# Kernel tuning notes

Measured on AMD Instinct MI355X. Metric: run time of the kernel, lower is better.

Reference implementation:

```python
import jax, jax.numpy as jnp
import numpy as np

CLS_NUM = 2
SCALE = 8.0
NO_OBJ_SCALE = 1.0
EPS = 1e-7


def setup_inputs() -> dict:
    key = jax.random.key(0)
    k1, k2, k3, k4, k5, k6 = jax.random.split(key, 6)
    B, C, H, W, N = 8, CLS_NUM, 512, 512, 160
    predict = jax.random.normal(k1, (B, C, H, W), dtype=jnp.float32)
    b = jax.random.randint(k2, (N,), 0, B).astype(jnp.float32)
    c = jax.random.randint(k3, (N,), 0, C).astype(jnp.float32)
    cxy = jax.random.uniform(k4, (N, 2), minval=0.0, maxval=H * SCALE)
    wh = jax.random.uniform(k5, (N, 2), minval=64.0, maxval=256.0)
    ang = jax.random.uniform(k6, (N, 1), minval=-np.pi, maxval=np.pi)
    targets = jnp.concatenate([b[:, None], c[:, None], cxy, wh, ang], axis=1).astype(jnp.float32)
    return {"predict": predict, "targets": targets}


def _forward(predict, targets):
    B, C, H, W = predict.shape
    pred = jnp.transpose(predict, (0, 2, 3, 1))          # [B,H,W,C]
    conf_all = jax.nn.sigmoid(pred)
    heatmap = jnp.max(conf_all, axis=-1)                 # [B,H,W]

    bid = targets[:, 0].astype(jnp.int32)                # [N] batch ids
    cid = targets[:, 1].astype(jnp.int32)                # [N] class ids
    cx = targets[:, 2] / SCALE
    cy = targets[:, 3] / SCALE
    w = targets[:, 4] / SCALE
    h = targets[:, 5] / SCALE
    ang = targets[:, 6]
    cos, sin = jnp.cos(ang), jnp.sin(ang)
    # rotate box center into the rotated frame (same math as render_map)
    x = cx * cos + cy * sin
    y = -cx * sin + cy * cos
    x3, x4 = x - h / 2, x + h / 2
    y3, y4 = y - w / 2, y + w / 2
    x1, x2 = x3 - 0.5, x4 + 0.5
    y1, y2 = y3 - 0.5, y4 + 0.5

    gx = jnp.arange(W, dtype=jnp.float32)[None, :] + 0.5  # [1,W] -> broadcasts to [H,W]
    gy = jnp.arange(H, dtype=jnp.float32)[:, None] + 0.5  # [H,1]
    vx = cos[:, None, None] * gx + sin[:, None, None] * gy   # [N,H,W]
    vy = -sin[:, None, None] * gx + cos[:, None, None] * gy  # [N,H,W]

    def box_mask(lo_x, hi_x, lo_y, hi_y):
        return ((lo_x[:, None, None] <= vx) & (vx <= hi_x[:, None, None]) &
                (lo_y[:, None, None] <= vy) & (vy <= hi_y[:, None, None]))

    inner = box_mask(x3, x4, y3, y4)  # obj region, [N,H,W]
    outer = box_mask(x1, x2, y1, y2)  # expanded region (clears noobj)

    loss = jnp.float32(0.0)
    for cls in range(CLS_NUM):
        sel = (cid == cls)[:, None, None]
        obj_cnt = jax.ops.segment_sum((inner & sel).astype(jnp.float32), bid, num_segments=B)
        out_cnt = jax.ops.segment_sum((outer & sel).astype(jnp.float32), bid, num_segments=B)
        obj_mask = obj_cnt > 0            # [B,H,W]
        noobj_mask = out_cnt <= 0         # starts at 1, zeroed inside any expanded box
        conf_c = jnp.clip(conf_all[..., cls], EPS, 1.0 - EPS)
        n_obj = jnp.sum(obj_mask)
        n_noobj = jnp.sum(noobj_mask)
        # BCE with target 1 on obj cells, target 0 on noobj cells (tconf == obj mask)
        loss_obj = -jnp.sum(jnp.where(obj_mask, jnp.log(conf_c), 0.0)) / jnp.maximum(n_obj, 1)
        loss_noobj = -jnp.sum(jnp.where(noobj_mask, jnp.log(1.0 - conf_c), 0.0)) / jnp.maximum(n_noobj, 1)
        loss = loss + jnp.where(n_obj > 0, loss_obj + NO_OBJ_SCALE * loss_noobj, 0.0)
    return loss, heatmap


def reference(predict, targets):
    return _forward(predict, targets)
```

## Files before the change

kernel.cpp:

```cpp
#include <hip/hip_runtime.h>
#include <math.h>

#define CLS 2
#define BATCH 8
#define HH 512
#define WW 512
#define INV_SCALE 0.125f
#define LOGEPS -16.118095651f

#define MAXT 256
#define NBLK 2048


__global__ __launch_bounds__(256) void heatmap_main(
    const float* __restrict__ predict, const float* __restrict__ targets,
    int nT, float* __restrict__ out,
    double* __restrict__ gsumd, int* __restrict__ gcnti)
{
    __shared__ float s_cs[MAXT], s_sn[MAXT], s_x3[MAXT], s_x4[MAXT],
                     s_y3[MAXT], s_y4[MAXT];
    __shared__ int s_cid[MAXT];
    __shared__ int s_nb;
    __shared__ double s_bs[4][4];
    __shared__ int s_bc[4][2];

    const int tid = threadIdx.x;
    const int blockPix = blockIdx.x << 10;
    const int b = blockPix >> 18;

    if (tid == 0) s_nb = 0;
    __syncthreads();
    for (int t0 = tid; t0 < nT; t0 += 256) {
        const float* tp = targets + t0 * 7;
        if ((int)tp[0] == b) {
            const float cs = cosf(tp[6]), sn = sinf(tp[6]);
            const float cx = tp[2] * INV_SCALE, cy = tp[3] * INV_SCALE;
            const float w_ = tp[4] * INV_SCALE, h_ = tp[5] * INV_SCALE;
            const float x =  cx * cs + cy * sn;
            const float y = -cx * sn + cy * cs;
            const int slot = atomicAdd(&s_nb, 1);
            s_cs[slot] = cs; s_sn[slot] = sn;
            s_x3[slot] = x - 0.5f * h_; s_x4[slot] = x + 0.5f * h_;
            s_y3[slot] = y - 0.5f * w_; s_y4[slot] = y + 0.5f * w_;
            s_cid[slot] = (int)tp[1];
        }
    }
    __syncthreads();
    const int nb = s_nb;

    const int wid = tid >> 6;
    const int l   = tid & 63;
    const int spix = blockPix + (wid << 8);
    const int i  = (spix >> 9) & (HH - 1);
    const int j0 = spix & (WW - 1);
    const float gy = (float)i + 0.5f;
    const int j = j0 + 4 * l;
    const float gxb = (float)j + 0.5f;

    int objm[4] = {0, 0, 0, 0}, outm[4] = {0, 0, 0, 0};

    for (int base = 0; base < nb; base += 64) {
        const int t = base + l;
        bool acc = false;
        if (t < nb) {
            const float cs = s_cs[t], sn = s_sn[t];
            const float gxl = (float)j0 + 0.5f, gxh = (float)j0 + 255.5f;
            const float a1 = cs * gxl + sn * gy, a2 = cs * gxh + sn * gy;
            const float b1 = -sn * gxl + cs * gy, b2 = -sn * gxh + cs * gy;
            const float vxlo = fminf(a1, a2), vxhi = fmaxf(a1, a2);
            const float vylo = fminf(b1, b2), vyhi = fmaxf(b1, b2);
            const float M = 0.51f;
            acc = (vxhi >= s_x3[t] - M) & (vxlo <= s_x4[t] + M) &
                  (vyhi >= s_y3[t] - M) & (vylo <= s_y4[t] + M);
        }
        unsigned long long bal = __ballot(acc);
        while (bal) {
            const int n = base + __builtin_ctzll(bal);
            bal &= bal - 1;
            const float ccs = s_cs[n], csn = s_sn[n];
            const float cx3 = s_x3[n], cx4 = s_x4[n];
            const float cy3 = s_y3[n], cy4 = s_y4[n];
            const int cbit = 1 << s_cid[n];
            float vx =  ccs * gxb + csn * gy;
            float vy = -csn * gxb + ccs * gy;
            #pragma unroll
            for (int k = 0; k < 4; ++k) {
                const bool in_  = (cx3 <= vx) & (vx <= cx4) &
                                  (cy3 <= vy) & (vy <= cy4);
                const bool out_ = (cx3 - 0.5f <= vx) & (vx <= cx4 + 0.5f) &
                                  (cy3 - 0.5f <= vy) & (vy <= cy4 + 0.5f);
                if (in_)  objm[k] |= cbit;
                if (out_) outm[k] |= cbit;
                vx += ccs; vy -= csn;
            }
        }
    }

    const int pbase = (b * CLS * HH + i) * WW + j;
    const float4 P0 = *(const float4*)(predict + pbase);
    const float4 P1 = *(const float4*)(predict + pbase + HH * WW);

    float so0 = 0.f, so1 = 0.f, sq0 = 0.f, sq1 = 0.f;
    int c_obj0 = 0, c_obj1 = 0, c_no0 = 0, c_no1 = 0;
    float hm[4];
    #pragma unroll
    for (int k = 0; k < 4; ++k) {
        const float p0 = (&P0.x)[k], p1 = (&P1.x)[k];
        const float t0 = __expf(p0), t1 = __expf(p1);
        const float l0n = -__logf(1.0f + t0);
        const float l1n = -__logf(1.0f + t1);
        const float lc0 = fmaxf(p0 + l0n, LOGEPS);
        const float lc1 = fmaxf(p1 + l1n, LOGEPS);
        const float l0c = fmaxf(l0n, LOGEPS);
        const float l1c = fmaxf(l1n, LOGEPS);
        const float tm = fmaxf(t0, t1);
        hm[k] = tm * __builtin_amdgcn_rcpf(1.0f + tm);
        const int om = objm[k], um = outm[k];
        if (om & 1) { so0 += lc0; ++c_obj0; }
        if (om & 2) { so1 += lc1; ++c_obj1; }
        if (!(um & 1)) { sq0 += l0c; ++c_no0; }
        if (!(um & 2)) { sq1 += l1c; ++c_no1; }
    }

    float* ho = out + 1 + (b * HH + i) * WW + j;
    ho[0] = hm[0]; ho[1] = hm[1]; ho[2] = hm[2]; ho[3] = hm[3];

    const unsigned long long anyobj =
        __ballot((objm[0] | objm[1] | objm[2] | objm[3]) != 0);
    int pc = (c_no0 & 0xffff) | (c_no1 << 16);
    #pragma unroll
    for (int off = 32; off >= 1; off >>= 1) {
        sq0 += __shfl_down(sq0, off);
        sq1 += __shfl_down(sq1, off);
        pc  += __shfl_down(pc, off);
    }
    int po = 0;
    if (anyobj) {
        po = (c_obj0 & 0xffff) | (c_obj1 << 16);
        #pragma unroll
        for (int off = 32; off >= 1; off >>= 1) {
            so0 += __shfl_down(so0, off);
            so1 += __shfl_down(so1, off);
            po  += __shfl_down(po, off);
        }
    }
    if (l == 0) {
        s_bs[wid][0] = (double)so0; s_bs[wid][1] = (double)so1;
        s_bs[wid][2] = (double)sq0; s_bs[wid][3] = (double)sq1;
        s_bc[wid][0] = po;          s_bc[wid][1] = pc;
    }
    __syncthreads();
    if (tid == 0) {
        double o0 = 0, o1 = 0, q0 = 0, q1 = 0;
        int P = 0, Q = 0;
        #pragma unroll
        for (int w = 0; w < 4; ++w) {
            o0 += s_bs[w][0]; o1 += s_bs[w][1];
            q0 += s_bs[w][2]; q1 += s_bs[w][3];
            P  += s_bc[w][0]; Q  += s_bc[w][1];
        }
        const int blk = blockIdx.x;
        gsumd[0 * NBLK + blk] = o0; gsumd[1 * NBLK + blk] = o1;
        gsumd[2 * NBLK + blk] = q0; gsumd[3 * NBLK + blk] = q1;
        gcnti[0 * NBLK + blk] = P;  gcnti[1 * NBLK + blk] = Q;
    }
}

__global__ __launch_bounds__(512) void heatmap_finalize(
    const double* __restrict__ gsumd, const int* __restrict__ gcnti,
    float* __restrict__ out)
{
    const int t = threadIdx.x;
    double f[4] = {0, 0, 0, 0};
    int co0 = 0, co1 = 0, cn0 = 0, cn1 = 0;
    for (int blk = t; blk < NBLK; blk += 512) {
        #pragma unroll
        for (int q = 0; q < 4; ++q) f[q] += gsumd[q * NBLK + blk];
        const int p = gcnti[0 * NBLK + blk];
        const int q2 = gcnti[1 * NBLK + blk];
        co0 += p & 0xffff;  co1 += p >> 16;
        cn0 += q2 & 0xffff; cn1 += q2 >> 16;
    }
    #pragma unroll
    for (int off = 32; off >= 1; off >>= 1) {
        #pragma unroll
        for (int q = 0; q < 4; ++q) f[q] += __shfl_down(f[q], off);
        co0 += __shfl_down(co0, off); co1 += __shfl_down(co1, off);
        cn0 += __shfl_down(cn0, off); cn1 += __shfl_down(cn1, off);
    }

    __shared__ double sf[8][4];
    __shared__ int    sc[8][4];
    const int wv = t >> 6, ln = t & 63;
    if (ln == 0) {
        #pragma unroll
        for (int q = 0; q < 4; ++q) sf[wv][q] = f[q];
        sc[wv][0] = co0; sc[wv][1] = co1; sc[wv][2] = cn0; sc[wv][3] = cn1;
    }
    __syncthreads();
    if (t == 0) {
        double F[4] = {0, 0, 0, 0}; int C[4] = {0, 0, 0, 0};
        for (int w = 0; w < 8; ++w)
            #pragma unroll
            for (int q = 0; q < 4; ++q) { F[q] += sf[w][q]; C[q] += sc[w][q]; }
        float loss = 0.0f;
        if (C[0] > 0)
            loss += -(float)F[0] / (float)C[0]
                    - (float)F[2] / (float)(C[2] > 0 ? C[2] : 1);
        if (C[1] > 0)
            loss += -(float)F[1] / (float)C[1]
                    - (float)F[3] / (float)(C[3] > 0 ? C[3] : 1);
        out[0] = loss;
    }
}

extern "C" void kernel_launch(void* const* d_in, const int* in_sizes, int n_in,
                              void* d_out, int out_size, void* d_ws, size_t ws_size,
                              hipStream_t stream) {
    const float* predict = (const float*)d_in[0];
    const float* targets = (const float*)d_in[1];
    const int nT = in_sizes[1] / 7;
    float* out = (float*)d_out;
    char* ws = (char*)d_ws;
    double* gsumd = (double*)ws;
    int* gcnti = (int*)(ws + 65536);

    heatmap_main<<<NBLK, 256, 0, stream>>>(predict, targets, nT, out,
                                           gsumd, gcnti);
    heatmap_finalize<<<1, 512, 0, stream>>>(gsumd, gcnti, out);
}
```

Measured before the change: 79.15 us.

## Fuse finalize into main kernel via cooperative grid sync; process 8 pixels per lane

Each block now covers 2048 pixels as four full rows, so a lane handles eight pixels and the grid shrinks to 1024 blocks. The box culling test runs per whole row instead of per half row. The noobj sum is now taken unconditionally and then corrected only for pixels inside any box, and log is computed with log2. When the device supports it, a cooperative launch with a grid sync lets block 0 do the final reduction, removing the second kernel launch. This relies on all 1024 blocks being co-resident at occupancy 4, pays for the grid barrier, and halves the block count, which may reduce latency hiding.

```diff
diff --git a/kernel.cpp b/kernel.cpp
--- a/kernel.cpp
+++ b/kernel.cpp
@@ -1,4 +1,5 @@
 #include <hip/hip_runtime.h>
+#include <hip/hip_cooperative_groups.h>
 #include <math.h>
 
 #define CLS 2
@@ -7,12 +8,16 @@
 #define WW 512
 #define INV_SCALE 0.125f
 #define LOGEPS -16.118095651f
-
-#define MAXT 256
-#define NBLK 2048
-
-
-__global__ __launch_bounds__(256) void heatmap_main(
+#define NLN2 -0.69314718056f
+
+#define MAXT 192
+#define NBLK 1024
+
+namespace cg = cooperative_groups;
+
+
+template <bool COOP>
+__global__ __launch_bounds__(256, 4) void heatmap_main(
     const float* __restrict__ predict, const float* __restrict__ targets,
     int nT, float* __restrict__ out,
     double* __restrict__ gsumd, int* __restrict__ gcnti)
@@ -22,10 +27,10 @@
     __shared__ int s_cid[MAXT];
     __shared__ int s_nb;
     __shared__ double s_bs[4][4];
-    __shared__ int s_bc[4][2];
+    __shared__ int s_bc[4][4];
 
     const int tid = threadIdx.x;
-    const int blockPix = blockIdx.x << 10;
+    const int blockPix = blockIdx.x << 11;
     const int b = blockPix >> 18;
 
     if (tid == 0) s_nb = 0;
@@ -48,25 +53,21 @@
     __syncthreads();
     const int nb = s_nb;
 
-    const int wid = tid >> 6;
-    const int l   = tid & 63;
-    const int spix = blockPix + (wid << 8);
-    const int i  = (spix >> 9) & (HH - 1);
-    const int j0 = spix & (WW - 1);
+    const int wid = tid >> 6, l = tid & 63;
+    const int i = ((blockPix >> 9) + wid) & (HH - 1);
     const float gy = (float)i + 0.5f;
-    const int j = j0 + 4 * l;
+    const int j = l << 3;
     const float gxb = (float)j + 0.5f;
 
-    int objm[4] = {0, 0, 0, 0}, outm[4] = {0, 0, 0, 0};
+    int objp = 0, outp = 0;
 
     for (int base = 0; base < nb; base += 64) {
         const int t = base + l;
         bool acc = false;
         if (t < nb) {
             const float cs = s_cs[t], sn = s_sn[t];
-            const float gxl = (float)j0 + 0.5f, gxh = (float)j0 + 255.5f;
-            const float a1 = cs * gxl + sn * gy, a2 = cs * gxh + sn * gy;
-            const float b1 = -sn * gxl + cs * gy, b2 = -sn * gxh + cs * gy;
+            const float a1 = cs * 0.5f + sn * gy,  a2 = cs * 511.5f + sn * gy;
+            const float b1 = -sn * 0.5f + cs * gy, b2 = -sn * 511.5f + cs * gy;
             const float vxlo = fminf(a1, a2), vxhi = fmaxf(a1, a2);
             const float vylo = fminf(b1, b2), vyhi = fmaxf(b1, b2);
             const float M = 0.51f;
@@ -80,54 +81,63 @@
             const float ccs = s_cs[n], csn = s_sn[n];
             const float cx3 = s_x3[n], cx4 = s_x4[n];
             const float cy3 = s_y3[n], cy4 = s_y4[n];
-            const int cbit = 1 << s_cid[n];
+            const float ox3 = cx3 - 0.5f, ox4 = cx4 + 0.5f;
+            const float oy3 = cy3 - 0.5f, oy4 = cy4 + 0.5f;
+            const int cb = 1 << s_cid[n];
             float vx =  ccs * gxb + csn * gy;
             float vy = -csn * gxb + ccs * gy;
             #pragma unroll
-            for (int k = 0; k < 4; ++k) {
+            for (int k = 0; k < 8; ++k) {
                 const bool in_  = (cx3 <= vx) & (vx <= cx4) &
                                   (cy3 <= vy) & (vy <= cy4);
-                const bool out_ = (cx3 - 0.5f <= vx) & (vx <= cx4 + 0.5f) &
-                                  (cy3 - 0.5f <= vy) & (vy <= cy4 + 0.5f);
-                if (in_)  objm[k] |= cbit;
-                if (out_) outm[k] |= cbit;
+                const bool out_ = (ox3 <= vx) & (vx <= ox4) &
+                                  (oy3 <= vy) & (vy <= oy4);
+                if (in_)  objp |= cb << (2 * k);
+                if (out_) outp |= cb << (2 * k);
                 vx += ccs; vy -= csn;
             }
         }
     }
 
     const int pbase = (b * CLS * HH + i) * WW + j;
-    const float4 P0 = *(const float4*)(predict + pbase);
-    const float4 P1 = *(const float4*)(predict + pbase + HH * WW);
-
-    float so0 = 0.f, so1 = 0.f, sq0 = 0.f, sq1 = 0.f;
-    int c_obj0 = 0, c_obj1 = 0, c_no0 = 0, c_no1 = 0;
-    float hm[4];
+    const float4 A0 = *(const float4*)(predict + pbase);
+    const float4 A1 = *(const float4*)(predict + pbase + 4);
+    const float4 B0 = *(const float4*)(predict + pbase + HH * WW);
+    const float4 B1 = *(const float4*)(predict + pbase + HH * WW + 4);
+    float p0[8], p1[8];
+    p0[0]=A0.x; p0[1]=A0.y; p0[2]=A0.z; p0[3]=A0.w;
+    p0[4]=A1.x; p0[5]=A1.y; p0[6]=A1.z; p0[7]=A1.w;
+    p1[0]=B0.x; p1[1]=B0.y; p1[2]=B0.z; p1[3]=B0.w;
+    p1[4]=B1.x; p1[5]=B1.y; p1[6]=B1.z; p1[7]=B1.w;
+
+    float l0n[8], l1n[8];
+    float sq0 = 0.f, sq1 = 0.f;
+    float* ho = out + 1 + (b * HH + i) * WW + j;
     #pragma unroll
-    for (int k = 0; k < 4; ++k) {
-        const float p0 = (&P0.x)[k], p1 = (&P1.x)[k];
-        const float t0 = __expf(p0), t1 = __expf(p1);
-        const float l0n = -__logf(1.0f + t0);
-        const float l1n = -__logf(1.0f + t1);
-        const float lc0 = fmaxf(p0 + l0n, LOGEPS);
-        const float lc1 = fmaxf(p1 + l1n, LOGEPS);
-        const float l0c = fmaxf(l0n, LOGEPS);
-        const float l1c = fmaxf(l1n, LOGEPS);
+    for (int k = 0; k < 8; ++k) {
+        const float t0 = __expf(p0[k]);
+        const float t1 = __expf(p1[k]);
+        l0n[k] = __log2f(1.0f + t0) * NLN2;
+        l1n[k] = __log2f(1.0f + t1) * NLN2;
+        sq0 += fmaxf(l0n[k], LOGEPS);
+        sq1 += fmaxf(l1n[k], LOGEPS);
         const float tm = fmaxf(t0, t1);
-        hm[k] = tm * __builtin_amdgcn_rcpf(1.0f + tm);
-        const int om = objm[k], um = outm[k];
-        if (om & 1) { so0 += lc0; ++c_obj0; }
-        if (om & 2) { so1 += lc1; ++c_obj1; }
-        if (!(um & 1)) { sq0 += l0c; ++c_no0; }
-        if (!(um & 2)) { sq1 += l1c; ++c_no1; }
-    }
-
-    float* ho = out + 1 + (b * HH + i) * WW + j;
-    ho[0] = hm[0]; ho[1] = hm[1]; ho[2] = hm[2]; ho[3] = hm[3];
-
-    const unsigned long long anyobj =
-        __ballot((objm[0] | objm[1] | objm[2] | objm[3]) != 0);
-    int pc = (c_no0 & 0xffff) | (c_no1 << 16);
+        ho[k] = tm * __builtin_amdgcn_rcpf(1.0f + tm);
+    }
+    int cn0 = 8, cn1 = 8, co0 = 0, co1 = 0;
+    float so0 = 0.f, so1 = 0.f;
+    if (outp) {
+        #pragma unroll
+        for (int k = 0; k < 8; ++k) {
+            if (outp & (1 << (2 * k))) { sq0 -= fmaxf(l0n[k], LOGEPS); --cn0; }
+            if (outp & (2 << (2 * k))) { sq1 -= fmaxf(l1n[k], LOGEPS); --cn1; }
+            if (objp & (1 << (2 * k))) { so0 += fmaxf(p0[k] + l0n[k], LOGEPS); ++co0; }
+            if (objp & (2 << (2 * k))) { so1 += fmaxf(p1[k] + l1n[k], LOGEPS); ++co1; }
+        }
+    }
+
+    const unsigned long long anyobj = __ballot(objp != 0);
+    int pc = (cn0 & 0xffff) | (cn1 << 16);
     #pragma unroll
     for (int off = 32; off >= 1; off >>= 1) {
         sq0 += __shfl_down(sq0, off);
@@ -136,7 +146,7 @@
     }
     int po = 0;
     if (anyobj) {
-        po = (c_obj0 & 0xffff) | (c_obj1 << 16);
+        po = (co0 & 0xffff) | (co1 << 16);
         #pragma unroll
         for (int off = 32; off >= 1; off >>= 1) {
             so0 += __shfl_down(so0, off);
@@ -163,46 +173,97 @@
         gsumd[0 * NBLK + blk] = o0; gsumd[1 * NBLK + blk] = o1;
         gsumd[2 * NBLK + blk] = q0; gsumd[3 * NBLK + blk] = q1;
         gcnti[0 * NBLK + blk] = P;  gcnti[1 * NBLK + blk] = Q;
+        __threadfence();
+    }
+
+    if (COOP) {
+        cg::this_grid().sync();
+        if (blockIdx.x == 0) {
+            __threadfence();
+            double f0 = 0, f1 = 0, f2 = 0, f3 = 0;
+            int c0 = 0, c1 = 0, c2 = 0, c3 = 0;
+            for (int blk = tid; blk < NBLK; blk += 256) {
+                f0 += gsumd[0 * NBLK + blk]; f1 += gsumd[1 * NBLK + blk];
+                f2 += gsumd[2 * NBLK + blk]; f3 += gsumd[3 * NBLK + blk];
+                const int P = gcnti[0 * NBLK + blk];
+                const int Q = gcnti[1 * NBLK + blk];
+                c0 += P & 0xffff; c1 += (int)((unsigned)P >> 16);
+                c2 += Q & 0xffff; c3 += (int)((unsigned)Q >> 16);
+            }
+            #pragma unroll
+            for (int off = 32; off >= 1; off >>= 1) {
+                f0 += __shfl_down(f0, off); f1 += __shfl_down(f1, off);
+                f2 += __shfl_down(f2, off); f3 += __shfl_down(f3, off);
+                c0 += __shfl_down(c0, off); c1 += __shfl_down(c1, off);
+                c2 += __shfl_down(c2, off); c3 += __shfl_down(c3, off);
+            }
+            const int wv = tid >> 6, ln = tid & 63;
+            if (ln == 0) {
+                s_bs[wv][0] = f0; s_bs[wv][1] = f1;
+                s_bs[wv][2] = f2; s_bs[wv][3] = f3;
+                s_bc[wv][0] = c0; s_bc[wv][1] = c1;
+                s_bc[wv][2] = c2; s_bc[wv][3] = c3;
+            }
+            __syncthreads();
+            if (tid == 0) {
+                double F[4] = {0, 0, 0, 0}; int C[4] = {0, 0, 0, 0};
+                for (int w = 0; w < 4; ++w) {
+                    F[0] += s_bs[w][0]; F[1] += s_bs[w][1];
+                    F[2] += s_bs[w][2]; F[3] += s_bs[w][3];
+                    C[0] += s_bc[w][0]; C[1] += s_bc[w][1];
+                    C[2] += s_bc[w][2]; C[3] += s_bc[w][3];
+                }
+                float loss = 0.0f;
+                if (C[0] > 0)
+                    loss += -(float)F[0] / (float)C[0]
+                            - (float)F[2] / (float)(C[2] > 0 ? C[2] : 1);
+                if (C[1] > 0)
+                    loss += -(float)F[1] / (float)C[1]
+                            - (float)F[3] / (float)(C[3] > 0 ? C[3] : 1);
+                out[0] = loss;
+            }
+        }
     }
 }
 
-__global__ __launch_bounds__(512) void heatmap_finalize(
+__global__ __launch_bounds__(256) void heatmap_finalize(
     const double* __restrict__ gsumd, const int* __restrict__ gcnti,
     float* __restrict__ out)
 {
+    __shared__ double sf[4][4];
+    __shared__ int    sc[4][4];
     const int t = threadIdx.x;
-    double f[4] = {0, 0, 0, 0};
-    int co0 = 0, co1 = 0, cn0 = 0, cn1 = 0;
-    for (int blk = t; blk < NBLK; blk += 512) {
-        #pragma unroll
-        for (int q = 0; q < 4; ++q) f[q] += gsumd[q * NBLK + blk];
-        const int p = gcnti[0 * NBLK + blk];
-        const int q2 = gcnti[1 * NBLK + blk];
-        co0 += p & 0xffff;  co1 += p >> 16;
-        cn0 += q2 & 0xffff; cn1 += q2 >> 16;
+    double f0 = 0, f1 = 0, f2 = 0, f3 = 0;
+    int c0 = 0, c1 = 0, c2 = 0, c3 = 0;
+    for (int blk = t; blk < NBLK; blk += 256) {
+        f0 += gsumd[0 * NBLK + blk]; f1 += gsumd[1 * NBLK + blk];
+        f2 += gsumd[2 * NBLK + blk]; f3 += gsumd[3 * NBLK + blk];
+        const int P = gcnti[0 * NBLK + blk];
+        const int Q = gcnti[1 * NBLK + blk];
+        c0 += P & 0xffff; c1 += (int)((unsigned)P >> 16);
+        c2 += Q & 0xffff; c3 += (int)((unsigned)Q >> 16);
     }
     #pragma unroll
     for (int off = 32; off >= 1; off >>= 1) {
-        #pragma unroll
-        for (int q = 0; q < 4; ++q) f[q] += __shfl_down(f[q], off);
-        co0 += __shfl_down(co0, off); co1 += __shfl_down(co1, off);
-        cn0 += __shfl_down(cn0, off); cn1 += __shfl_down(cn1, off);
-    }
-
-    __shared__ double sf[8][4];
-    __shared__ int    sc[8][4];
+        f0 += __shfl_down(f0, off); f1 += __shfl_down(f1, off);
+        f2 += __shfl_down(f2, off); f3 += __shfl_down(f3, off);
+        c0 += __shfl_down(c0, off); c1 += __shfl_down(c1, off);
+        c2 += __shfl_down(c2, off); c3 += __shfl_down(c3, off);
+    }
     const int wv = t >> 6, ln = t & 63;
     if (ln == 0) {
-        #pragma unroll
-        for (int q = 0; q < 4; ++q) sf[wv][q] = f[q];
-        sc[wv][0] = co0; sc[wv][1] = co1; sc[wv][2] = cn0; sc[wv][3] = cn1;
+        sf[wv][0] = f0; sf[wv][1] = f1; sf[wv][2] = f2; sf[wv][3] = f3;
+        sc[wv][0] = c0; sc[wv][1] = c1; sc[wv][2] = c2; sc[wv][3] = c3;
     }
     __syncthreads();
     if (t == 0) {
         double F[4] = {0, 0, 0, 0}; int C[4] = {0, 0, 0, 0};
-        for (int w = 0; w < 8; ++w)
-            #pragma unroll
-            for (int q = 0; q < 4; ++q) { F[q] += sf[w][q]; C[q] += sc[w][q]; }
+        for (int w = 0; w < 4; ++w) {
+            F[0] += sf[w][0]; F[1] += sf[w][1];
+            F[2] += sf[w][2]; F[3] += sf[w][3];
+            C[0] += sc[w][0]; C[1] += sc[w][1];
+            C[2] += sc[w][2]; C[3] += sc[w][3];
+        }
         float loss = 0.0f;
         if (C[0] > 0)
             loss += -(float)F[0] / (float)C[0]
@@ -217,15 +278,41 @@
 extern "C" void kernel_launch(void* const* d_in, const int* in_sizes, int n_in,
                               void* d_out, int out_size, void* d_ws, size_t ws_size,
                               hipStream_t stream) {
+    (void)n_in; (void)out_size; (void)ws_size;
     const float* predict = (const float*)d_in[0];
     const float* targets = (const float*)d_in[1];
     const int nT = in_sizes[1] / 7;
     float* out = (float*)d_out;
     char* ws = (char*)d_ws;
     double* gsumd = (double*)ws;
-    int* gcnti = (int*)(ws + 65536);
-
-    heatmap_main<<<NBLK, 256, 0, stream>>>(predict, targets, nT, out,
-                                           gsumd, gcnti);
-    heatmap_finalize<<<1, 512, 0, stream>>>(gsumd, gcnti, out);
+    int* gcnti = (int*)(ws + 32768);
+
+    static int coop_ok = -1;
+    if (coop_ok < 0) {
+        int perCU = 0;
+        hipError_t e = hipOccupancyMaxActiveBlocksPerMultiprocessor(
+            &perCU, reinterpret_cast<const void*>(&heatmap_main<true>), 256, 0);
+        int dev = 0, nCU = 0, coopAttr = 0;
+        hipGetDevice(&dev);
+        hipDeviceGetAttribute(&nCU, hipDeviceAttributeMultiprocessorCount, dev);
+        hipDeviceGetAttribute(&coopAttr, hipDeviceAttributeCooperativeLaunch, dev);
+        coop_ok = (e == hipSuccess && coopAttr != 0 &&
+                   (long)perCU * (long)nCU >= NBLK) ? 1 : 0;
+    }
+
+    bool done = false;
+    if (coop_ok == 1) {
+        void* args[] = {(void*)&predict, (void*)&targets, (void*)&nT,
+                        (void*)&out, (void*)&gsumd, (void*)&gcnti};
+        hipError_t e = hipLaunchCooperativeKernel(
+            reinterpret_cast<const void*>(&heatmap_main<true>),
+            dim3(NBLK), dim3(256), args, 0, stream);
+        if (e == hipSuccess) done = true;
+        else coop_ok = 0;
+    }
+    if (!done) {
+        heatmap_main<false><<<NBLK, 256, 0, stream>>>(predict, targets, nT, out,
+                                                      gsumd, gcnti);
+        heatmap_finalize<<<1, 256, 0, stream>>>(gsumd, gcnti, out);
+    }
 }
```

Measured after the change: 214.6 us. 2.71x slower.
